# Performance work log

Hardware: AMD Instinct MI355X
Metric: run time of the kernel (lower is better)

Reference implementation:

```python
import math
import jax, jax.numpy as jnp
import numpy as np

N_EMBD = 1024
N_HEAD = 16
EPS = 1e-5


def get_alibi_slopes(n_head):
    def pow2_slopes(n):
        start = 2 ** (-2 ** (-(math.log2(n) - 3)))
        return [start * start ** i for i in range(n)]
    if math.log2(n_head).is_integer():
        slopes = pow2_slopes(n_head)
    else:
        c = 2 ** math.floor(math.log2(n_head))
        slopes = pow2_slopes(c)
        extra = pow2_slopes(2 * c)[0::2]
        slopes.extend(extra[: n_head - c])
    return jnp.asarray(slopes, dtype=jnp.float32)


def layernorm(x, w, b):
    mu = jnp.mean(x, axis=-1, keepdims=True)
    var = jnp.var(x, axis=-1, keepdims=True)
    return (x - mu) * jax.lax.rsqrt(var + EPS) * w + b


def setup_inputs() -> dict:
    key = jax.random.key(0)
    ks = jax.random.split(key, 8)
    C = N_EMBD
    B, T = 2, 2048
    s = 0.02
    return {
        "x": jax.random.normal(ks[0], (B, T, C), dtype=jnp.float32),
        "ln1_w": jnp.ones((C,), jnp.float32),
        "ln1_b": jnp.zeros((C,), jnp.float32),
        "w_qkv": jax.random.normal(ks[1], (C, 3 * C), dtype=jnp.float32) * s,
        "b_qkv": jnp.zeros((3 * C,), jnp.float32),
        "w_proj": jax.random.normal(ks[2], (C, C), dtype=jnp.float32) * s,
        "b_proj": jnp.zeros((C,), jnp.float32),
        "ln2_w": jnp.ones((C,), jnp.float32),
        "ln2_b": jnp.zeros((C,), jnp.float32),
        "w_fc": jax.random.normal(ks[3], (C, 4 * C), dtype=jnp.float32) * s,
        "b_fc": jnp.zeros((4 * C,), jnp.float32),
        "w_fc2": jax.random.normal(ks[4], (4 * C, C), dtype=jnp.float32) * s,
        "b_fc2": jnp.zeros((C,), jnp.float32),
    }


def reference(x, ln1_w, ln1_b, w_qkv, b_qkv, w_proj, b_proj,
              ln2_w, ln2_b, w_fc, b_fc, w_fc2, b_fc2):
    B, T, C = x.shape
    H = N_HEAD
    D = C // H

    # --- attention with ALiBi ---
    h = layernorm(x, ln1_w, ln1_b)
    qkv = h @ w_qkv + b_qkv                       # [B,T,3C]
    q, k, v = jnp.split(qkv, 3, axis=-1)
    q = q.reshape(B, T, H, D).transpose(0, 2, 1, 3)  # [B,H,T,D]
    k = k.reshape(B, T, H, D).transpose(0, 2, 1, 3)
    v = v.reshape(B, T, H, D).transpose(0, 2, 1, 3)

    att = jnp.einsum('bhqd,bhkd->bhqk', q, k) * (1.0 / math.sqrt(D))

    pos = jnp.arange(T, dtype=jnp.float32)
    distances = pos[:, None] - pos[None, :]        # [T,T], i-j
    slopes = get_alibi_slopes(H)[:, None, None]     # [H,1,1]
    bias = slopes * distances[None, :, :]           # [H,T,T]
    causal = jnp.triu(jnp.ones((T, T), dtype=bool), k=1)
    bias = jnp.where(causal[None, :, :], -jnp.inf, bias)

    att = jax.nn.softmax(att + bias[None], axis=-1)
    y = jnp.einsum('bhqk,bhkd->bhqd', att, v)
    y = y.transpose(0, 2, 1, 3).reshape(B, T, C)
    x = x + y @ w_proj + b_proj

    # --- MLP ---
    h = layernorm(x, ln2_w, ln2_b)
    h = jax.nn.gelu(h @ w_fc + b_fc, approximate=False)
    x = x + h @ w_fc2 + b_fc2
    return x
```

## Files before the change

### kernel.cpp

```cpp
#include <hip/hip_runtime.h>
#include <hip/hip_bf16.h>
#include <math.h>

#define N_EMBD 1024
#define N_HEADC 16
#define HEAD_D 64

typedef __attribute__((ext_vector_type(8))) short short8;
typedef __attribute__((ext_vector_type(4))) float floatx4;

__device__ __forceinline__ ushort f2b(float f) {
    __hip_bfloat16 h = __float2bfloat16(f);
    return *reinterpret_cast<ushort*>(&h);
}

__device__ __forceinline__ void async_cp16(const void* gsrc, void* ldst) {
    __builtin_amdgcn_global_load_lds(
        (const __attribute__((address_space(1))) void*)gsrc,
        (__attribute__((address_space(3))) void*)ldst, 16, 0, 0);
}

__device__ __forceinline__ int xcd_swizzle(int bid, int nwg) {
    const int q = nwg >> 3, r = nwg & 7;
    const int xcd = bid & 7, loc = bid >> 3;
    return (xcd < r ? xcd * (q + 1) : r * (q + 1) + (xcd - r) * q) + loc;
}

template <int CTRL>
__device__ __forceinline__ float dppf(float x) {
    int r = __builtin_amdgcn_update_dpp(0, __builtin_bit_cast(int, x),
                                        CTRL, 0xF, 0xF, true);
    return __builtin_bit_cast(float, r);
}
__device__ __forceinline__ float redmax16(float x) {
    x = fmaxf(x, dppf<0xB1>(x));
    x = fmaxf(x, dppf<0x4E>(x));
    x = fmaxf(x, dppf<0x141>(x));
    x = fmaxf(x, dppf<0x140>(x));
    return x;
}
__device__ __forceinline__ float redsum16(float x) {
    x += dppf<0xB1>(x);
    x += dppf<0x4E>(x);
    x += dppf<0x141>(x);
    x += dppf<0x140>(x);
    return x;
}

__global__ __launch_bounds__(256) void ln_kernel(const float* __restrict__ x,
                                                 const float* __restrict__ w,
                                                 const float* __restrict__ b,
                                                 ushort* __restrict__ out) {
    const int row = blockIdx.x;
    const int t = threadIdx.x;
    const float4 v = reinterpret_cast<const float4*>(x + (size_t)row * N_EMBD)[t];
    float s  = v.x + v.y + v.z + v.w;
    float ss = v.x * v.x + v.y * v.y + v.z * v.z + v.w * v.w;
    for (int o = 32; o > 0; o >>= 1) {
        s  += __shfl_down(s, o);
        ss += __shfl_down(ss, o);
    }
    __shared__ float as_[4], ass_[4];
    const int wid = t >> 6, lane = t & 63;
    if (lane == 0) { as_[wid] = s; ass_[wid] = ss; }
    __syncthreads();
    const float ts  = as_[0] + as_[1] + as_[2] + as_[3];
    const float tss = ass_[0] + ass_[1] + ass_[2] + ass_[3];
    const float mu  = ts * (1.f / N_EMBD);
    const float var = tss * (1.f / N_EMBD) - mu * mu;
    const float inv = rsqrtf(var + 1e-5f);
    const float4 wv = reinterpret_cast<const float4*>(w)[t];
    const float4 bv = reinterpret_cast<const float4*>(b)[t];
    ushort4 o;
    o.x = f2b((v.x - mu) * inv * wv.x + bv.x);
    o.y = f2b((v.y - mu) * inv * wv.y + bv.y);
    o.z = f2b((v.z - mu) * inv * wv.z + bv.z);
    o.w = f2b((v.w - mu) * inv * wv.w + bv.w);
    reinterpret_cast<ushort4*>(out + (size_t)row * N_EMBD)[t] = o;
}

__global__ void convtrans_kernel(const float* __restrict__ W,
                                 ushort* __restrict__ Wt, int K, int N) {
    __shared__ float tile[32][33];
    const int tid = threadIdx.x;
    const int r = tid >> 3;
    const int c4 = (tid & 7) * 4;
    const int bx = blockIdx.x, by = blockIdx.y;

    float4 v = *(const float4*)&W[((size_t)(by * 32 + r)) * N + bx * 32 + c4];
    tile[r][c4 + 0] = v.x; tile[r][c4 + 1] = v.y;
    tile[r][c4 + 2] = v.z; tile[r][c4 + 3] = v.w;
    __syncthreads();

    ushort4 u;
    u.x = f2b(tile[c4 + 0][r]); u.y = f2b(tile[c4 + 1][r]);
    u.z = f2b(tile[c4 + 2][r]); u.w = f2b(tile[c4 + 3][r]);
    *(ushort4*)&Wt[((size_t)(bx * 32 + r)) * K + by * 32 + c4] = u;
}

__device__ __forceinline__ void gemm_stage(
        const ushort* __restrict__ A, const ushort* __restrict__ Bt,
        ushort* As, ushort* Bs,
        int m0, int n0, int K, int k0, int w, int lane) {
#pragma unroll
    for (int l = 0; l < 2; l++) {
        const int cbase = w * 128 + l * 64;
        const int c = cbase + lane;
        const int row = c >> 2, kc8 = (c & 3) * 8;
        async_cp16(A  + (size_t)(m0 + row) * K + k0 + kc8, &As[cbase * 8]);
        async_cp16(Bt + (size_t)(n0 + row) * K + k0 + kc8, &Bs[cbase * 8]);
    }
}

__device__ __forceinline__ void gemm_compute(
        const ushort* As, const ushort* Bs, floatx4 (*acc)[4],
        int wm, int wn, int quad, int l16) {
    short8 a[4], bf[4];
#pragma unroll
    for (int i = 0; i < 4; i++)
        a[i] = *(const short8*)&As[(wm * 64 + i * 16 + l16) * 32 + quad * 8];
#pragma unroll
    for (int j = 0; j < 4; j++)
        bf[j] = *(const short8*)&Bs[(wn * 64 + j * 16 + l16) * 32 + quad * 8];
#pragma unroll
    for (int i = 0; i < 4; i++)
#pragma unroll
        for (int j = 0; j < 4; j++)
            acc[i][j] = __builtin_amdgcn_mfma_f32_16x16x32_bf16(
                a[i], bf[j], acc[i][j], 0, 0, 0);
}

__global__ __launch_bounds__(256) void gemm_bf16_kernel(
        const ushort* __restrict__ A,
        const ushort* __restrict__ Bt,
        const float* __restrict__ bias,
        const float* __restrict__ residual,
        float* __restrict__ out32,
        ushort* __restrict__ out16,
        int M, int N, int K, int do_gelu) {
    __shared__ ushort As[2][128 * 32];
    __shared__ ushort Bs[2][128 * 32];

    const int tid  = threadIdx.x;
    const int w    = tid >> 6;
    const int lane = tid & 63;
    const int quad = lane >> 4;
    const int l16  = lane & 15;
    const int wm   = w >> 1;
    const int wn   = w & 1;

    int bid = blockIdx.y * gridDim.x + blockIdx.x;
    bid = xcd_swizzle(bid, gridDim.x * gridDim.y);
    const int bx = bid % gridDim.x;
    const int by = bid / gridDim.x;
    const int m0 = by * 128;
    const int n0 = bx * 128;

    floatx4 acc[4][4];
#pragma unroll
    for (int i = 0; i < 4; i++)
#pragma unroll
        for (int j = 0; j < 4; j++) acc[i][j] = (floatx4){0.f, 0.f, 0.f, 0.f};

    const int nt = K >> 5;

    gemm_stage(A, Bt, As[0], Bs[0], m0, n0, K, 0, w, lane);
    __syncthreads();

    for (int t = 0; t < nt; t += 2) {
        gemm_stage(A, Bt, As[1], Bs[1], m0, n0, K, (t + 1) << 5, w, lane);
        gemm_compute(As[0], Bs[0], acc, wm, wn, quad, l16);
        __syncthreads();
        if (t + 2 < nt)
            gemm_stage(A, Bt, As[0], Bs[0], m0, n0, K, (t + 2) << 5, w, lane);
        gemm_compute(As[1], Bs[1], acc, wm, wn, quad, l16);
        __syncthreads();
    }

#pragma unroll
    for (int i = 0; i < 4; i++) {
#pragma unroll
        for (int j = 0; j < 4; j++) {
            const int nn = n0 + wn * 64 + j * 16 + l16;
            const float bv = bias[nn];
#pragma unroll
            for (int r = 0; r < 4; r++) {
                const int mm = m0 + wm * 64 + i * 16 + quad * 4 + r;
                float v = acc[i][j][r] + bv;
                if (do_gelu) v = 0.5f * v * (1.f + erff(v * 0.70710678118654752f));
                if (residual) v += residual[(size_t)mm * N + nn];
                if (out32) out32[(size_t)mm * N + nn] = v;
                if (out16) out16[(size_t)mm * N + nn] = f2b(v);
            }
        }
    }
}

#define AT_PAD 72
#define LOG2E 1.4426950408889634f

__device__ __forceinline__ void attn_tile_step(
        short8 aq0, short8 aq1,
        ushort (*__restrict__ Ks)[AT_PAD],
        ushort (*__restrict__ Vt)[AT_PAD],
        ushort (*__restrict__ Ps)[AT_PAD],
        float* m_r, float* l_r, floatx4* acc,
        int q0, int kt, bool domask,
        float qs2, float slope2, const float* skb,
        int w, int quad, int l16) {
    floatx4 sfrag[4];
#pragma unroll
    for (int kb = 0; kb < 4; kb++) {
        const int kcol = kb * 16 + l16;
        short8 bk0 = *(const short8*)&Ks[kcol][quad * 8];
        short8 bk1 = *(const short8*)&Ks[kcol][32 + quad * 8];
        floatx4 s = (floatx4){0.f, 0.f, 0.f, 0.f};
        s = __builtin_amdgcn_mfma_f32_16x16x32_bf16(aq0, bk0, s, 0, 0, 0);
        s = __builtin_amdgcn_mfma_f32_16x16x32_bf16(aq1, bk1, s, 0, 0, 0);
        sfrag[kb] = s;
    }

    const int psw = ((w * 4 + quad) & 7) << 3;
    int pcol[4];
#pragma unroll
    for (int kb = 0; kb < 4; kb++) pcol[kb] = (kb * 16 + l16) ^ psw;

    const float ktb = (float)(kt * 64);
#pragma unroll
    for (int r = 0; r < 4; r++) {
        const int q = q0 + w * 16 + quad * 4 + r;
        const float rowc = slope2 * ((float)q - ktb);
        float sv[4];
        float rm = -INFINITY;
#pragma unroll
        for (int kb = 0; kb < 4; kb++) {
            float s = fmaf(sfrag[kb][r], qs2, rowc) - skb[kb];
            if (domask) {
                const int k = kt * 64 + kb * 16 + l16;
                s = (k <= q) ? s : -INFINITY;
            }
            sv[kb] = s;
            rm = fmaxf(rm, s);
        }
        rm = redmax16(rm);
        if (rm > m_r[r]) {
            const float corr = exp2f(m_r[r] - rm);
            m_r[r] = rm;
            l_r[r] *= corr;
#pragma unroll
            for (int db = 0; db < 4; db++) acc[db][r] *= corr;
        }
        float rs = 0.f;
#pragma unroll
        for (int kb = 0; kb < 4; kb++) {
            const float pv = exp2f(sv[kb] - m_r[r]);
            rs += pv;
            Ps[w * 16 + quad * 4 + r][pcol[kb]] = f2b(pv);
        }
        rs = redsum16(rs);
        l_r[r] += rs;
    }

    const int prw = ((w * 4 + (l16 >> 2)) & 7) << 3;
    short8 ap0 = *(const short8*)&Ps[w * 16 + l16][(quad * 8) ^ prw];
    short8 ap1 = *(const short8*)&Ps[w * 16 + l16][(32 + quad * 8) ^ prw];
#pragma unroll
    for (int db = 0; db < 4; db++) {
        const int dv = db * 16 + l16;
        const int svw = ((db * 4 + (l16 >> 2)) & 7) << 3;
        short8 bv0 = *(const short8*)&Vt[dv][(quad * 8) ^ svw];
        short8 bv1 = *(const short8*)&Vt[dv][(32 + quad * 8) ^ svw];
        acc[db] = __builtin_amdgcn_mfma_f32_16x16x32_bf16(ap0, bv0, acc[db], 0, 0, 0);
        acc[db] = __builtin_amdgcn_mfma_f32_16x16x32_bf16(ap1, bv1, acc[db], 0, 0, 0);
    }
}

__global__ __launch_bounds__(256) void attn_mfma_kernel(
        const ushort* __restrict__ qkv, ushort* __restrict__ y, int B, int T) {
    const int C3 = 3 * N_EMBD;
    const int NT = T / 64;

    const int gx = gridDim.x, gxy = gridDim.x * gridDim.y;
    int lin = blockIdx.z * gxy + blockIdx.y * gx + blockIdx.x;
    lin = xcd_swizzle(lin, gxy * gridDim.z);
    const int p = lin % gx;
    const int h = (lin / gx) % gridDim.y;
    const int b = lin / gxy;

    const int qt = NT - 1 - p;
    const int tid  = threadIdx.x;
    const int lane = tid & 63;
    const int w    = tid >> 6;
    const int quad = lane >> 4;
    const int l16  = lane & 15;

    __shared__ ushort Qs[64][AT_PAD];
    __shared__ ushort Ks[64][AT_PAD];
    __shared__ ushort Vt[64][AT_PAD];
    __shared__ ushort Ps[64][AT_PAD];

    const float slope  = exp2f(-0.5f * (float)(h + 1));
    const float slope2 = slope * LOG2E;
    const float qs2    = 0.125f * LOG2E;
    float skb[4];
#pragma unroll
    for (int kb = 0; kb < 4; kb++) skb[kb] = slope2 * (float)(kb * 16 + l16);

    const int q0 = qt * 64;
    const size_t hb = (size_t)b * T * C3 + (size_t)h * HEAD_D;

#pragma unroll
    for (int i = 0; i < 4; i++) {
        int idx = tid + i * 256;
        int row = idx >> 4, d0 = (idx & 15) * 4;
        *(ushort4*)&Qs[row][d0] =
            *(const ushort4*)&qkv[hb + (size_t)(q0 + row) * C3 + d0];
    }
    __syncthreads();

    const int mrow = w * 16 + l16;
    short8 aq0 = *(const short8*)&Qs[mrow][quad * 8];
    short8 aq1 = *(const short8*)&Qs[mrow][32 + quad * 8];

    float m_r[4], l_r[4];
    floatx4 acc[4];
#pragma unroll
    for (int r = 0; r < 4; r++) {
        m_r[r] = -INFINITY; l_r[r] = 0.f;
        acc[r] = (floatx4){0.f, 0.f, 0.f, 0.f};
    }

    for (int kt = 0; kt <= qt; kt++) {
#pragma unroll
        for (int i = 0; i < 4; i++) {
            int idx = tid + i * 256;
            int row = idx >> 4, d0 = (idx & 15) * 4;
            const size_t src = hb + (size_t)(kt * 64 + row) * C3 + d0;
            *(ushort4*)&Ks[row][d0] = *(const ushort4*)&qkv[src + N_EMBD];
            ushort4 vv = *(const ushort4*)&qkv[src + 2 * N_EMBD];
            const int rs = row ^ ((idx & 7) << 3);
            Vt[d0 + 0][rs] = vv.x;
            Vt[d0 + 1][rs] = vv.y;
            Vt[d0 + 2][rs] = vv.z;
            Vt[d0 + 3][rs] = vv.w;
        }
        __syncthreads();

        attn_tile_step(aq0, aq1, Ks, Vt, Ps, m_r, l_r, acc,
                       q0, kt, kt == qt, qs2, slope2, skb, w, quad, l16);
        __syncthreads();
    }

#pragma unroll
    for (int r = 0; r < 4; r++) {
        const int qa = q0 + w * 16 + quad * 4 + r;
        const float ia = 1.f / l_r[r];
#pragma unroll
        for (int db = 0; db < 4; db++) {
            y[((size_t)b * T + qa) * N_EMBD + h * HEAD_D + db * 16 + l16] =
                f2b(acc[db][r] * ia);
        }
    }
}

extern "C" void kernel_launch(void* const* d_in, const int* in_sizes, int n_in,
                              void* d_out, int out_size, void* d_ws, size_t ws_size,
                              hipStream_t stream) {
    const int B = 2, T = 2048, C = N_EMBD;
    const int M = B * T;

    const float* x      = (const float*)d_in[0];
    const float* ln1_w  = (const float*)d_in[1];
    const float* ln1_b  = (const float*)d_in[2];
    const float* w_qkv  = (const float*)d_in[3];
    const float* b_qkv  = (const float*)d_in[4];
    const float* w_proj = (const float*)d_in[5];
    const float* b_proj = (const float*)d_in[6];
    const float* ln2_w  = (const float*)d_in[7];
    const float* ln2_b  = (const float*)d_in[8];
    const float* w_fc   = (const float*)d_in[9];
    const float* b_fc   = (const float*)d_in[10];
    const float* w_fc2  = (const float*)d_in[11];
    const float* b_fc2  = (const float*)d_in[12];
    float* out = (float*)d_out;

    char* ws = (char*)d_ws;
    size_t off = 0;
    ushort* wt_qkv  = (ushort*)(ws + off); off += (size_t)3 * C * C * 2;
    ushort* wt_proj = (ushort*)(ws + off); off += (size_t)C * C * 2;
    ushort* wt_fc   = (ushort*)(ws + off); off += (size_t)4 * C * C * 2;
    ushort* wt_fc2  = (ushort*)(ws + off); off += (size_t)4 * C * C * 2;
    ushort* h16     = (ushort*)(ws + off); off += (size_t)M * C * 2;
    ushort* qkv16   = (ushort*)(ws + off); off += (size_t)M * 3 * C * 2;
    ushort* y16     = (ushort*)(ws + off); off += (size_t)M * C * 2;
    ushort* fc16    = (ushort*)(ws + off); off += (size_t)M * 4 * C * 2;

    convtrans_kernel<<<dim3(3 * C / 32, C / 32), 256, 0, stream>>>(w_qkv, wt_qkv, C, 3 * C);
    convtrans_kernel<<<dim3(C / 32, C / 32), 256, 0, stream>>>(w_proj, wt_proj, C, C);
    convtrans_kernel<<<dim3(4 * C / 32, C / 32), 256, 0, stream>>>(w_fc, wt_fc, C, 4 * C);
    convtrans_kernel<<<dim3(C / 32, 4 * C / 32), 256, 0, stream>>>(w_fc2, wt_fc2, 4 * C, C);

    ln_kernel<<<M, 256, 0, stream>>>(x, ln1_w, ln1_b, h16);

    gemm_bf16_kernel<<<dim3(3 * C / 128, M / 128), 256, 0, stream>>>(
        h16, wt_qkv, b_qkv, nullptr, nullptr, qkv16, M, 3 * C, C, 0);

    attn_mfma_kernel<<<dim3(T / 64, N_HEADC, B), 256, 0, stream>>>(
        qkv16, y16, B, T);

    gemm_bf16_kernel<<<dim3(C / 128, M / 128), 256, 0, stream>>>(
        y16, wt_proj, b_proj, x, out, nullptr, M, C, C, 0);

    ln_kernel<<<M, 256, 0, stream>>>(out, ln2_w, ln2_b, h16);

    gemm_bf16_kernel<<<dim3(4 * C / 128, M / 128), 256, 0, stream>>>(
        h16, wt_fc, b_fc, nullptr, nullptr, fc16, M, 4 * C, C, 1);

    gemm_bf16_kernel<<<dim3(C / 128, M / 128), 256, 0, stream>>>(
        fc16, wt_fc2, b_fc2, out, out, nullptr, M, C, 4 * C, 0);
}
```

Measured before the change: 466.7 us.

## Split the fc2 GEMM over K into two partials and combine in a separate kernel

The fc2 GEMM (K=4096, N=1024) now runs with a z-dimension of 2, so each block handles half of the K range. Each half writes an fp32 partial buffer, and a new combine kernel sums the two partials and adds the bias and the residual. The aim is to double the number of workgroups for a GEMM whose 128x128 tiling otherwise gives only about one block per CU, improving occupancy and latency hiding. The cost is writing and reading two full fp32 partial buffers plus one extra launch. The partials reuse the h16 scratch buffer, which may be too small if it was sized for bf16 data.

```diff
diff --git a/kernel.cpp b/kernel.cpp
--- a/kernel.cpp
+++ b/kernel.cpp
@@ -156,23 +156,28 @@
     const int m0 = by * 128;
     const int n0 = bx * 128;
 
+    const int kchunk = K / gridDim.z;
+    const int kbeg   = blockIdx.z * kchunk;
+    if (gridDim.z > 1)
+        out32 += (size_t)blockIdx.z * M * N;
+
     floatx4 acc[4][4];
 #pragma unroll
     for (int i = 0; i < 4; i++)
 #pragma unroll
         for (int j = 0; j < 4; j++) acc[i][j] = (floatx4){0.f, 0.f, 0.f, 0.f};
 
-    const int nt = K >> 5;
-
-    gemm_stage(A, Bt, As[0], Bs[0], m0, n0, K, 0, w, lane);
+    const int nt = kchunk >> 5;
+
+    gemm_stage(A, Bt, As[0], Bs[0], m0, n0, K, kbeg, w, lane);
     __syncthreads();
 
     for (int t = 0; t < nt; t += 2) {
-        gemm_stage(A, Bt, As[1], Bs[1], m0, n0, K, (t + 1) << 5, w, lane);
+        gemm_stage(A, Bt, As[1], Bs[1], m0, n0, K, kbeg + ((t + 1) << 5), w, lane);
         gemm_compute(As[0], Bs[0], acc, wm, wn, quad, l16);
         __syncthreads();
         if (t + 2 < nt)
-            gemm_stage(A, Bt, As[0], Bs[0], m0, n0, K, (t + 2) << 5, w, lane);
+            gemm_stage(A, Bt, As[0], Bs[0], m0, n0, K, kbeg + ((t + 2) << 5), w, lane);
         gemm_compute(As[1], Bs[1], acc, wm, wn, quad, l16);
         __syncthreads();
     }
@@ -182,7 +187,7 @@
 #pragma unroll
         for (int j = 0; j < 4; j++) {
             const int nn = n0 + wn * 64 + j * 16 + l16;
-            const float bv = bias[nn];
+            const float bv = bias ? bias[nn] : 0.f;
 #pragma unroll
             for (int r = 0; r < 4; r++) {
                 const int mm = m0 + wm * 64 + i * 16 + quad * 4 + r;
@@ -194,6 +199,21 @@
             }
         }
     }
+}
+
+__global__ __launch_bounds__(256) void combine_kernel(
+        const float* __restrict__ p0, const float* __restrict__ p1,
+        const float* __restrict__ bias, float* __restrict__ out) {
+    const int i = blockIdx.x * 256 + threadIdx.x;
+    const float4 a = ((const float4*)p0)[i];
+    const float4 c = ((const float4*)p1)[i];
+    const float4 bb = ((const float4*)bias)[i & 255];
+    float4 o = ((float4*)out)[i];
+    o.x += a.x + c.x + bb.x;
+    o.y += a.y + c.y + bb.y;
+    o.z += a.z + c.z + bb.z;
+    o.w += a.w + c.w + bb.w;
+    ((float4*)out)[i] = o;
 }
 
 #define AT_PAD 72
@@ -416,6 +436,9 @@
     gemm_bf16_kernel<<<dim3(4 * C / 128, M / 128), 256, 0, stream>>>(
         h16, wt_fc, b_fc, nullptr, nullptr, fc16, M, 4 * C, C, 1);
 
-    gemm_bf16_kernel<<<dim3(C / 128, M / 128), 256, 0, stream>>>(
-        fc16, wt_fc2, b_fc2, out, out, nullptr, M, C, 4 * C, 0);
-}
+    float* part = (float*)h16;
+    gemm_bf16_kernel<<<dim3(C / 128, M / 128, 2), 256, 0, stream>>>(
+        fc16, wt_fc2, nullptr, nullptr, part, nullptr, M, C, 4 * C, 0);
+    combine_kernel<<<(M * C) / (256 * 4), 256, 0, stream>>>(
+        part, part + (size_t)M * C, b_fc2, out);
+}
```

Measured after the change: 440.9 us. 5.5% less time.
